# Optimization experiments

Measured on AMD Instinct MI355X. Metric: run time of the kernel, lower is better.

## Reference

```python
import jax, jax.numpy as jnp
import numpy as np

B, N, K = 8, 16384, 32
EPS = 1e-5


def setup_inputs() -> dict:
    key = jax.random.key(0)
    ks = jax.random.split(key, 11)
    xyz = jax.random.normal(ks[0], (B, N, 3), jnp.float32)
    intensity = jax.random.normal(ks[1], (B, 3, N), jnp.float32)
    indices = jax.random.randint(ks[2], (B, N, K), 0, N)
    # linear_p: Conv2d(3,3,1)+BN+ReLU, then Conv2d(3,1,1)
    w1 = jax.random.normal(ks[3], (3, 3), jnp.float32) * 0.3
    b1 = jax.random.normal(ks[4], (3,), jnp.float32) * 0.1
    gamma = jax.random.uniform(ks[5], (3,), jnp.float32, 0.5, 1.5)
    beta = jax.random.normal(ks[6], (3,), jnp.float32) * 0.1
    mean = jax.random.normal(ks[7], (3,), jnp.float32) * 0.1
    var = jax.random.uniform(ks[8], (3,), jnp.float32, 0.5, 1.5)
    w2 = jax.random.normal(ks[9], (1, 3), jnp.float32) * 0.3
    b2 = jax.random.normal(ks[10], (1,), jnp.float32) * 0.1
    return dict(xyz=xyz, intensity=intensity, indices=indices, w1=w1, b1=b1,
                gamma=gamma, beta=beta, mean=mean, var=var, w2=w2, b2=b2)


def reference(xyz, intensity, indices, w1, b1, gamma, beta, mean, var, w2, b2):
    # neighbor gathers (irregular access)
    xyz_nb = jax.vmap(lambda p, i: p[i])(xyz, indices)          # [B,N,K,3]
    i_nb = jax.vmap(lambda ft, i: ft[:, i])(intensity, indices)  # [B,3,N,K]
    # relative position + gaussian kernel
    pos = xyz_nb - xyz[:, :, None, :]                            # [B,N,K,3]
    pos_g = jnp.exp(-2.0 * pos * pos)
    pos_g = jnp.transpose(pos_g, (0, 3, 1, 2))                   # [B,3,N,K]
    # 1x1 conv (3->3) + eval-mode BN + ReLU
    h = jnp.einsum('oc,bcnk->bonk', w1, pos_g) + b1[None, :, None, None]
    scale = gamma / jnp.sqrt(var + EPS)
    h = (h - mean[None, :, None, None]) * scale[None, :, None, None] + beta[None, :, None, None]
    h = jax.nn.relu(h)
    # 1x1 conv (3->1), softmax over neighbors
    w = jnp.einsum('oc,bcnk->bonk', w2, h) + b2[None, :, None, None]  # [B,1,N,K]
    w = jax.nn.softmax(w, axis=-1)
    # weighted reduce over neighbors
    return jnp.sum(i_nb * w, axis=-1)                            # [B,3,N]
```

## Files before the change

kernel.cpp:

```cpp
#include <hip/hip_runtime.h>
#include <hip/hip_fp16.h>
#include <math.h>

#define PB 8
#define PN 16384
#define PK 32
#define PEPS 1e-5f

template <int CTRL>
__device__ __forceinline__ float dpp_add_step(float v) {
    int t = __builtin_amdgcn_update_dpp(0, __float_as_int(v), CTRL, 0xf, 0xf, true);
    return v + __int_as_float(t);
}
__device__ __forceinline__ float reduce32_to_lane31(float v) {
    v = dpp_add_step<0x111>(v);
    v = dpp_add_step<0x112>(v);
    v = dpp_add_step<0x114>(v);
    v = dpp_add_step<0x118>(v);
    v = dpp_add_step<0x142>(v);
    return v;
}

__global__ __launch_bounds__(256) void sa_pack(
    const float* __restrict__ xyz,
    const float* __restrict__ intensity,
    uint4* __restrict__ packed,
    const float* __restrict__ w1, const float* __restrict__ b1,
    const float* __restrict__ gamma_, const float* __restrict__ beta_,
    const float* __restrict__ mean_, const float* __restrict__ var_,
    const float* __restrict__ w2, const float* __restrict__ b2,
    float* __restrict__ cst)
{
    const int t = blockIdx.x * 256 + threadIdx.x;
    const int b = t >> 14;
    const int n = t & (PN - 1);
    const float x = xyz[(long)t * 3 + 0];
    const float y = xyz[(long)t * 3 + 1];
    const float z = xyz[(long)t * 3 + 2];
    const float* ib = intensity + (long)b * 3 * PN;
    const float i0 = ib[0 * PN + n];
    const float i1 = ib[1 * PN + n];
    const float i2 = ib[2 * PN + n];

    union { __half2 h2[4]; uint4 u; } rec;
    const __half hz = __float2half_rn(z);
    rec.h2[0] = __halves2half2(__float2half_rn(x), __float2half_rn(y));
    rec.h2[1] = __halves2half2(hz, __float2half_rn(0.f));
    rec.h2[2] = __halves2half2(__float2half_rn(i0), __float2half_rn(i1));
    rec.h2[3] = __halves2half2(__float2half_rn(i2), __float2half_rn(0.f));
    packed[t] = rec.u;

    if (t == 0) {
        for (int o = 0; o < 3; ++o) {
            const float sc = gamma_[o] * rsqrtf(var_[o] + PEPS);
            for (int c = 0; c < 3; ++c) cst[o * 3 + c] = w1[o * 3 + c] * sc;
            cst[9 + o]  = (b1[o] - mean_[o]) * sc + beta_[o];
            cst[12 + o] = w2[o];
        }
        cst[15] = b2[0];
    }
}

__global__ __launch_bounds__(256) void sa_main(
    const uint4* __restrict__ packed,
    const int*   __restrict__ indices,
    const float* __restrict__ cst,
    float* __restrict__ out)
{
    const int lane = threadIdx.x & 31;
    const int grp  = threadIdx.x >> 5;
    const int ng   = blockIdx.x * 8 + grp;
    const int b = ng >> 14;
    const int n = ng & (PN - 1);

    const float A00 = cst[0], A01 = cst[1], A02 = cst[2];
    const float A10 = cst[3], A11 = cst[4], A12 = cst[5];
    const float A20 = cst[6], A21 = cst[7], A22 = cst[8];
    const float d0 = cst[9], d1 = cst[10], d2 = cst[11];
    const float w0 = cst[12], w1v = cst[13], w2v = cst[14];
    const float bias2 = cst[15];

    const uint4 c = packed[ng];
    const float2 cxy = __half22float2(*(const __half2*)&c.x);
    const float  cz  = __half2float(*(const __half*)&c.y);

    const int idx = indices[(long)ng * PK + lane];
    const uint4 r = packed[(b << 14) | idx];

    const float2 nxy = __half22float2(*(const __half2*)&r.x);
    const float  nz  = __half2float(*(const __half*)&r.y);
    const float2 ni01 = __half22float2(*(const __half2*)&r.z);
    const float  ni2  = __half2float(*(const __half*)&r.w);

    const float px = nxy.x - cxy.x;
    const float py = nxy.y - cxy.y;
    const float pz = nz - cz;

    const float g0 = __expf(-2.f * px * px);
    const float g1 = __expf(-2.f * py * py);
    const float g2 = __expf(-2.f * pz * pz);

    float h0 = fmaf(A00, g0, fmaf(A01, g1, fmaf(A02, g2, d0)));
    float h1 = fmaf(A10, g0, fmaf(A11, g1, fmaf(A12, g2, d1)));
    float h2 = fmaf(A20, g0, fmaf(A21, g1, fmaf(A22, g2, d2)));
    h0 = fmaxf(h0, 0.f); h1 = fmaxf(h1, 0.f); h2 = fmaxf(h2, 0.f);
    const float logit = fmaf(w0, h0, fmaf(w1v, h1, fmaf(w2v, h2, bias2)));

    const float e = __expf(logit);

    float s  = reduce32_to_lane31(e);
    float a0 = reduce32_to_lane31(e * ni01.x);
    float a1 = reduce32_to_lane31(e * ni01.y);
    float a2 = reduce32_to_lane31(e * ni2);

    if (lane == 31) {
        const float inv = 1.f / s;
        float* ob = out + (long)b * 3 * PN;
        ob[0 * PN + n] = a0 * inv;
        ob[1 * PN + n] = a1 * inv;
        ob[2 * PN + n] = a2 * inv;
    }
}

__global__ __launch_bounds__(256) void sa_fallback(
    const float* __restrict__ xyz, const float* __restrict__ intensity,
    const int* __restrict__ indices,
    const float* __restrict__ w1, const float* __restrict__ b1,
    const float* __restrict__ gamma_, const float* __restrict__ beta_,
    const float* __restrict__ mean_, const float* __restrict__ var_,
    const float* __restrict__ w2, const float* __restrict__ b2,
    float* __restrict__ out)
{
    const int lane = threadIdx.x & 31;
    const int grp  = threadIdx.x >> 5;
    const long ng  = (long)blockIdx.x * 8 + grp;
    const int b = (int)(ng >> 14);
    const int n = (int)(ng & (PN - 1));

    float A[3][3], d[3], wv[3];
#pragma unroll
    for (int o = 0; o < 3; ++o) {
        const float sc = gamma_[o] * rsqrtf(var_[o] + PEPS);
#pragma unroll
        for (int c = 0; c < 3; ++c) A[o][c] = w1[o * 3 + c] * sc;
        d[o]  = (b1[o] - mean_[o]) * sc + beta_[o];
        wv[o] = w2[o];
    }
    const float bias2 = b2[0];
    const long bn = (long)b * PN + n;
    const float cx = xyz[bn * 3 + 0], cy = xyz[bn * 3 + 1], cz = xyz[bn * 3 + 2];
    const int idx = indices[bn * PK + lane];
    const long bi = (long)b * PN + idx;
    const float px = xyz[bi * 3 + 0] - cx;
    const float py = xyz[bi * 3 + 1] - cy;
    const float pz = xyz[bi * 3 + 2] - cz;
    const float g0 = __expf(-2.f * px * px);
    const float g1 = __expf(-2.f * py * py);
    const float g2 = __expf(-2.f * pz * pz);
    float logit = bias2;
#pragma unroll
    for (int o = 0; o < 3; ++o) {
        float h = A[o][0] * g0 + A[o][1] * g1 + A[o][2] * g2 + d[o];
        h = fmaxf(h, 0.f);
        logit = fmaf(wv[o], h, logit);
    }
    float m = logit;
#pragma unroll
    for (int s = 16; s > 0; s >>= 1) m = fmaxf(m, __shfl_xor(m, s, 64));
    const float e = __expf(logit - m);
    const float* ib = intensity + (long)b * 3 * PN;
    float ssum = e;
    float a0 = e * ib[0 * PN + idx];
    float a1 = e * ib[1 * PN + idx];
    float a2 = e * ib[2 * PN + idx];
#pragma unroll
    for (int s = 16; s > 0; s >>= 1) {
        ssum += __shfl_xor(ssum, s, 64);
        a0 += __shfl_xor(a0, s, 64);
        a1 += __shfl_xor(a1, s, 64);
        a2 += __shfl_xor(a2, s, 64);
    }
    if (lane == 0) {
        const float inv = 1.f / ssum;
        float* ob = out + (long)b * 3 * PN;
        ob[0 * PN + n] = a0 * inv;
        ob[1 * PN + n] = a1 * inv;
        ob[2 * PN + n] = a2 * inv;
    }
}

extern "C" void kernel_launch(void* const* d_in, const int* in_sizes, int n_in,
                              void* d_out, int out_size, void* d_ws, size_t ws_size,
                              hipStream_t stream) {
    const float* xyz       = (const float*)d_in[0];
    const float* intensity = (const float*)d_in[1];
    const int*   indices   = (const int*)d_in[2];
    const float* w1        = (const float*)d_in[3];
    const float* b1        = (const float*)d_in[4];
    const float* gamma_    = (const float*)d_in[5];
    const float* beta_     = (const float*)d_in[6];
    const float* mean_     = (const float*)d_in[7];
    const float* var_      = (const float*)d_in[8];
    const float* w2        = (const float*)d_in[9];
    const float* b2        = (const float*)d_in[10];
    float* out = (float*)d_out;

    const int points = PB * PN;
    const size_t rec_bytes = (size_t)points * 16;
    const size_t need = rec_bytes + 64;

    if (ws_size >= need) {
        uint4* packed = (uint4*)d_ws;
        float* cst = (float*)((char*)d_ws + rec_bytes);
        sa_pack<<<points / 256, 256, 0, stream>>>(xyz, intensity, packed,
                                                  w1, b1, gamma_, beta_, mean_,
                                                  var_, w2, b2, cst);
        sa_main<<<points / 8, 256, 0, stream>>>(packed, indices, cst, out);
    } else {
        sa_fallback<<<points / 8, 256, 0, stream>>>(xyz, intensity, indices, w1, b1,
                                                    gamma_, beta_, mean_, var_, w2, b2, out);
    }
}
```

Baseline: 115.5 us.

## Process each point with 4 lanes handling 8 neighbors each

The main kernel now assigns 4 threads per output point instead of 32, with each thread loading 8 neighbor indices through two int4 loads and gathering 8 packed records. Each thread accumulates softmax numerator and denominator serially, and a 2-step quad DPP reduction replaces the 5-step 32-lane reduction. The three outputs are written by three different lanes. This cuts reduction and per-thread overhead and raises memory-level parallelism per thread, at the cost of more registers and fewer waves overall.

```diff
diff --git a/kernel.cpp b/kernel.cpp
--- a/kernel.cpp
+++ b/kernel.cpp
@@ -8,16 +8,13 @@
 #define PEPS 1e-5f
 
 template <int CTRL>
-__device__ __forceinline__ float dpp_add_step(float v) {
+__device__ __forceinline__ float quad_add_step(float v) {
     int t = __builtin_amdgcn_update_dpp(0, __float_as_int(v), CTRL, 0xf, 0xf, true);
     return v + __int_as_float(t);
 }
-__device__ __forceinline__ float reduce32_to_lane31(float v) {
-    v = dpp_add_step<0x111>(v);
-    v = dpp_add_step<0x112>(v);
-    v = dpp_add_step<0x114>(v);
-    v = dpp_add_step<0x118>(v);
-    v = dpp_add_step<0x142>(v);
+__device__ __forceinline__ float quad_reduce(float v) {
+    v = quad_add_step<0xB1>(v);
+    v = quad_add_step<0x4E>(v);
     return v;
 }
 
@@ -43,9 +40,8 @@
     const float i2 = ib[2 * PN + n];
 
     union { __half2 h2[4]; uint4 u; } rec;
-    const __half hz = __float2half_rn(z);
     rec.h2[0] = __halves2half2(__float2half_rn(x), __float2half_rn(y));
-    rec.h2[1] = __halves2half2(hz, __float2half_rn(0.f));
+    rec.h2[1] = __halves2half2(__float2half_rn(z), __float2half_rn(0.f));
     rec.h2[2] = __halves2half2(__float2half_rn(i0), __float2half_rn(i1));
     rec.h2[3] = __halves2half2(__float2half_rn(i2), __float2half_rn(0.f));
     packed[t] = rec.u;
@@ -61,17 +57,17 @@
     }
 }
 
-__global__ __launch_bounds__(256) void sa_main(
+__global__ __launch_bounds__(256) void sa_main4(
     const uint4* __restrict__ packed,
     const int*   __restrict__ indices,
     const float* __restrict__ cst,
     float* __restrict__ out)
 {
-    const int lane = threadIdx.x & 31;
-    const int grp  = threadIdx.x >> 5;
-    const int ng   = blockIdx.x * 8 + grp;
-    const int b = ng >> 14;
-    const int n = ng & (PN - 1);
+    const int t = blockIdx.x * 256 + threadIdx.x;
+    const int q = t >> 2;
+    const int l = t & 3;
+    const int b = q >> 14;
+    const int n = q & (PN - 1);
 
     const float A00 = cst[0], A01 = cst[1], A02 = cst[2];
     const float A10 = cst[3], A11 = cst[4], A12 = cst[5];
@@ -80,45 +76,57 @@
     const float w0 = cst[12], w1v = cst[13], w2v = cst[14];
     const float bias2 = cst[15];
 
-    const uint4 c = packed[ng];
+    const uint4 c = packed[q];
     const float2 cxy = __half22float2(*(const __half2*)&c.x);
     const float  cz  = __half2float(*(const __half*)&c.y);
 
-    const int idx = indices[(long)ng * PK + lane];
-    const uint4 r = packed[(b << 14) | idx];
-
-    const float2 nxy = __half22float2(*(const __half2*)&r.x);
-    const float  nz  = __half2float(*(const __half*)&r.y);
-    const float2 ni01 = __half22float2(*(const __half2*)&r.z);
-    const float  ni2  = __half2float(*(const __half*)&r.w);
-
-    const float px = nxy.x - cxy.x;
-    const float py = nxy.y - cxy.y;
-    const float pz = nz - cz;
-
-    const float g0 = __expf(-2.f * px * px);
-    const float g1 = __expf(-2.f * py * py);
-    const float g2 = __expf(-2.f * pz * pz);
-
-    float h0 = fmaf(A00, g0, fmaf(A01, g1, fmaf(A02, g2, d0)));
-    float h1 = fmaf(A10, g0, fmaf(A11, g1, fmaf(A12, g2, d1)));
-    float h2 = fmaf(A20, g0, fmaf(A21, g1, fmaf(A22, g2, d2)));
-    h0 = fmaxf(h0, 0.f); h1 = fmaxf(h1, 0.f); h2 = fmaxf(h2, 0.f);
-    const float logit = fmaf(w0, h0, fmaf(w1v, h1, fmaf(w2v, h2, bias2)));
-
-    const float e = __expf(logit);
-
-    float s  = reduce32_to_lane31(e);
-    float a0 = reduce32_to_lane31(e * ni01.x);
-    float a1 = reduce32_to_lane31(e * ni01.y);
-    float a2 = reduce32_to_lane31(e * ni2);
-
-    if (lane == 31) {
-        const float inv = 1.f / s;
-        float* ob = out + (long)b * 3 * PN;
-        ob[0 * PN + n] = a0 * inv;
-        ob[1 * PN + n] = a1 * inv;
-        ob[2 * PN + n] = a2 * inv;
+    const int4* ip = (const int4*)(indices + (long)q * PK + l * 8);
+    const int4 i0v = ip[0];
+    const int4 i1v = ip[1];
+    int idxs[8] = { i0v.x, i0v.y, i0v.z, i0v.w, i1v.x, i1v.y, i1v.z, i1v.w };
+
+    uint4 rec[8];
+#pragma unroll
+    for (int j = 0; j < 8; ++j) rec[j] = packed[(b << 14) | idxs[j]];
+
+    float s = 0.f, a0 = 0.f, a1 = 0.f, a2 = 0.f;
+#pragma unroll
+    for (int j = 0; j < 8; ++j) {
+        const uint4 r = rec[j];
+        const float2 nxy  = __half22float2(*(const __half2*)&r.x);
+        const float  nz   = __half2float(*(const __half*)&r.y);
+        const float2 ni01 = __half22float2(*(const __half2*)&r.z);
+        const float  ni2  = __half2float(*(const __half*)&r.w);
+
+        const float px = nxy.x - cxy.x;
+        const float py = nxy.y - cxy.y;
+        const float pz = nz - cz;
+
+        const float g0 = __expf(-2.f * px * px);
+        const float g1 = __expf(-2.f * py * py);
+        const float g2 = __expf(-2.f * pz * pz);
+
+        float h0 = fmaf(A00, g0, fmaf(A01, g1, fmaf(A02, g2, d0)));
+        float h1 = fmaf(A10, g0, fmaf(A11, g1, fmaf(A12, g2, d1)));
+        float h2 = fmaf(A20, g0, fmaf(A21, g1, fmaf(A22, g2, d2)));
+        h0 = fmaxf(h0, 0.f); h1 = fmaxf(h1, 0.f); h2 = fmaxf(h2, 0.f);
+        const float logit = fmaf(w0, h0, fmaf(w1v, h1, fmaf(w2v, h2, bias2)));
+
+        const float e = __expf(logit);
+        s += e;
+        a0 = fmaf(e, ni01.x, a0);
+        a1 = fmaf(e, ni01.y, a1);
+        a2 = fmaf(e, ni2,    a2);
+    }
+
+    s  = quad_reduce(s);
+    a0 = quad_reduce(a0);
+    a1 = quad_reduce(a1);
+    a2 = quad_reduce(a2);
+
+    if (l < 3) {
+        const float val = (l == 0) ? a0 : ((l == 1) ? a1 : a2);
+        out[(long)b * 3 * PN + l * PN + n] = val * (1.f / s);
     }
 }
 
@@ -215,7 +223,7 @@
         sa_pack<<<points / 256, 256, 0, stream>>>(xyz, intensity, packed,
                                                   w1, b1, gamma_, beta_, mean_,
                                                   var_, w2, b2, cst);
-        sa_main<<<points / 8, 256, 0, stream>>>(packed, indices, cst, out);
+        sa_main4<<<(points * 4) / 256, 256, 0, stream>>>(packed, indices, cst, out);
     } else {
         sa_fallback<<<points / 8, 256, 0, stream>>>(xyz, intensity, indices, w1, b1,
                                                     gamma_, beta_, mean_, var_, w2, b2, out);
```

Result: slower. 125.3 us (+8.6%).
